# Kernel optimization log

Measured on AMD Instinct MI355X. Metric: run time of the kernel, lower is better.

The kernel has to match this reference:

```python
import jax, jax.numpy as jnp
import numpy as np

N, E, IN, ED, H, C = 50000, 800000, 128, 32, 4, 32
HC = H * C
SCALE = 1.0 / float(np.sqrt(C))


def _seg_softmax(t, idx, n):
    # t: [E, H], idx: [E] target-node ids -> per-segment softmax over incoming edges
    m = jax.ops.segment_max(t, idx, num_segments=n)
    m = jnp.where(jnp.isfinite(m), m, 0.0)
    e = jnp.exp(t - m[idx])
    z = jax.ops.segment_sum(e, idx, num_segments=n)
    return e / (z[idx] + 1e-16)


def setup_inputs() -> dict:
    key = jax.random.key(0)
    ks = jax.random.split(key, 26)
    w = lambda k, shape: (jax.random.normal(k, shape, jnp.float32) * 0.05)
    return {
        "x": jax.random.normal(ks[0], (N, IN), jnp.float32),
        "edge_index": jax.random.randint(ks[1], (2, E), 0, N),
        "edge_attr": jax.random.normal(ks[2], (E, ED), jnp.float32),
        # DifferentialGraphAttention params (dual QK groups + lambda)
        "Wq1": w(ks[3], (HC, IN)), "Wq2": w(ks[4], (HC, IN)),
        "Wk1": w(ks[5], (HC, IN)), "Wk2": w(ks[6], (HC, IN)),
        "Wvd": w(ks[7], (HC, IN)),
        "Wkr1": w(ks[8], (HC, ED)), "Wkr2": w(ks[9], (HC, ED)),
        "Wvrd": w(ks[10], (HC, ED)),
        "Woutd": w(ks[11], (HC, HC)),
        "lam": jnp.float32(0.8),
        # RelationActivationAttention params
        "Wqa": w(ks[12], (HC, IN)), "Wka": w(ks[13], (HC, IN)), "Wva": w(ks[14], (HC, IN)),
        "Wkra": w(ks[15], (HC, ED)), "Wvra": w(ks[16], (HC, ED)),
        "Wouta": w(ks[17], (HC, HC)),
        # Hybrid fusion params
        "Wproj": w(ks[18], (HC, 2 * HC)), "bproj": jnp.zeros((HC,), jnp.float32),
        "Win": w(ks[19], (HC, IN)), "b_in": jnp.zeros((HC,), jnp.float32),
        "rms_w": jnp.ones((HC,), jnp.float32),
    }


def reference(x, edge_index, edge_attr, Wq1, Wq2, Wk1, Wk2, Wvd, Wkr1, Wkr2, Wvrd,
              Woutd, lam, Wqa, Wka, Wva, Wkra, Wvra, Wouta, Wproj, bproj, Win, b_in,
              rms_w):
    src, dst = edge_index[0], edge_index[1]

    def nproj(W):  # [N, HC] -> [N, H, C]
        return (x @ W.T).reshape(N, H, C)

    def eproj(W):  # [E, HC] -> [E, H, C]
        return (edge_attr @ W.T).reshape(E, H, C)

    # ---- differential relation aggregation branch ----
    Q1, Q2, K1, K2, Vd = nproj(Wq1), nproj(Wq2), nproj(Wk1), nproj(Wk2), nproj(Wvd)
    t1 = jnp.sum(Q1[dst] * (K1[src] + eproj(Wkr1)), axis=-1) * SCALE  # [E, H]
    t2 = jnp.sum(Q2[dst] * (K2[src] + eproj(Wkr2)), axis=-1) * SCALE
    a_diff = _seg_softmax(t1, dst, N) - lam * _seg_softmax(t2, dst, N)
    msg_d = (Vd[src] + eproj(Wvrd)) * a_diff[..., None]               # [E, H, C]
    h_aggr = jax.ops.segment_sum(msg_d, dst, num_segments=N).reshape(N, HC) @ Woutd.T

    # ---- relation activation branch ----
    Qa, Ka, Va = nproj(Wqa), nproj(Wka), nproj(Wva)
    ta = jnp.sum(Qa[dst] * (Ka[src] + eproj(Wkra)), axis=-1) * SCALE  # [E, H]
    a_act = _seg_softmax(ta, dst, N)
    msg_a = (Va[src] + eproj(Wvra)) * a_act[..., None]
    h_actv = jax.ops.segment_sum(msg_a, dst, num_segments=N).reshape(N, HC) @ Wouta.T

    # ---- hybrid fusion + residual + RMSNorm ----
    h = jnp.concatenate([h_aggr, h_actv], axis=-1) @ Wproj.T + bproj
    h = h + (x @ Win.T + b_in)
    h = h * jax.lax.rsqrt(jnp.mean(h * h, axis=-1, keepdims=True) + 1e-6) * rms_w
    return h
```

## Files before the change

kernel.cpp:

```cpp
#include <hip/hip_runtime.h>

typedef unsigned short u16;
typedef unsigned int   u32;
typedef _Float16 half8 __attribute__((ext_vector_type(8)));
typedef _Float16 half2v __attribute__((ext_vector_type(2)));
typedef float    f32x4 __attribute__((ext_vector_type(4)));
typedef unsigned int u32x4 __attribute__((ext_vector_type(4)));
typedef int      i32x2 __attribute__((ext_vector_type(2)));

#define NN 50000
#define EE 800000
#define SCALE 0.17677669529663687f
#define NB 49

#define O_WNODET   0ul
#define O_WFT      393216ul
#define O_WF1      524288ul
#define O_WF3      589824ul
#define O_HIST     655360ul
#define O_BSUM     855360ul
#define O_BOFF     855616ul
#define O_OFF      856064ul
#define O_CUR      1056768ul
#define O_PERM     1257472ul
#define O_NODEQ    7657472ul
#define O_NODEKV   97257472ul
#define O_G        161257472ul

__device__ __forceinline__ float fin(float x){
  return (x == x && fabsf(x) < 3e38f) ? x : 0.f;
}
__device__ __forceinline__ u32 packh(float a, float b){
  union{ u32 u; _Float16 h[2]; } cv; cv.h[0]=(_Float16)a; cv.h[1]=(_Float16)b; return cv.u;
}
union H2U { u32 u; half2v h; };
__device__ __forceinline__ half2v h2(u32 u){ H2U c; c.u=u; return c.h; }

__device__ __forceinline__ u32x4 ntl4(const u32* p){
  return __builtin_nontemporal_load((const u32x4*)p);
}
__device__ __forceinline__ f32x4 ntlf4(const float* p){
  return __builtin_nontemporal_load((const f32x4*)p);
}
__device__ __forceinline__ i32x2 ntl2(const i32x2* p){
  return __builtin_nontemporal_load(p);
}

__global__ __launch_bounds__(256) void xcast(const float* __restrict__ x,
                                             _Float16* __restrict__ xh)
{
  int i = blockIdx.x*256 + threadIdx.x;
  size_t b = (size_t)i * 8;
  float4 v0 = *(const float4*)(x + b);
  float4 v1 = *(const float4*)(x + b + 4);
  half8 h;
  h[0]=(_Float16)v0.x; h[1]=(_Float16)v0.y; h[2]=(_Float16)v0.z; h[3]=(_Float16)v0.w;
  h[4]=(_Float16)v1.x; h[5]=(_Float16)v1.y; h[6]=(_Float16)v1.z; h[7]=(_Float16)v1.w;
  *(half8*)(xh + b) = h;
}

__global__ __launch_bounds__(256) void prep1(
    const float* __restrict__ Wq1, const float* __restrict__ Wq2, const float* __restrict__ Wqa,
    const float* __restrict__ Wk1, const float* __restrict__ Wk2, const float* __restrict__ Wka,
    const float* __restrict__ Wvd, const float* __restrict__ Wva, const float* __restrict__ Win,
    const float* __restrict__ Wkr1, const float* __restrict__ Wkr2, const float* __restrict__ Wkra,
    const float* __restrict__ Wproj, const float* __restrict__ Woutd, const float* __restrict__ Wouta,
    _Float16* __restrict__ WnodeT, float* __restrict__ Wf1, float* __restrict__ Wf3)
{
  int job = blockIdx.x*256 + threadIdx.x;
  if (job < 1536*128) {
    int n = job >> 7, kk = job & 127;
    int slot = n >> 7, o = n & 127;
    float val;
    if (slot==3 || slot==4 || slot==5) {
      const float* Wkr = (slot==3)?Wkr1:(slot==4)?Wkr2:Wkra;
      const float* Wq  = (slot==3)?Wq1 :(slot==4)?Wq2 :Wqa;
      int h=o>>5, j=o&31;
      float s=0.f;
      for (int c=0;c<32;c++)
        s += Wkr[(h*32+c)*32 + j] * Wq[(h*32+c)*128 + kk];
      val = s;
    } else {
      const float* W = (slot==0)?Wq1:(slot==1)?Wq2:(slot==2)?Wqa:
                       (slot==6)?Wk1:(slot==7)?Wk2:(slot==8)?Wka:
                       (slot==9)?Wvd:(slot==10)?Wva:Win;
      val = W[o*128 + kk];
    }
    WnodeT[n*128 + kk] = (_Float16)fin(val);
  } else {
    int idx = job - 1536*128;
    int which = idx >> 14;
    int r = idx & 16383;
    int o = r >> 7, v = r & 127;
    const float* Wout = which ? Wouta : Woutd;
    float s=0.f;
    for (int u=0;u<128;u++)
      s += Wproj[o*256 + which*128 + u] * Wout[u*128 + v];
    (which?Wf3:Wf1)[o*128+v] = fin(s);
  }
}

__global__ __launch_bounds__(256) void prep2(
    const float* __restrict__ Wf1, const float* __restrict__ Wf3,
    const float* __restrict__ Wvrd, const float* __restrict__ Wvra,
    _Float16* __restrict__ WfT)
{
  int job = blockIdx.x*256 + threadIdx.x;
  int o = job >> 9, kk = job & 511;
  int seg = kk >> 7, v = kk & 127;
  float val;
  if (seg==0) val = Wf1[o*128+v];
  else if (seg==2) val = Wf3[o*128+v];
  else {
    const float* Wf = (seg==1)?Wf1:Wf3;
    const float* Wv = (seg==1)?Wvrd:Wvra;
    int h=v>>5, j=v&31; float s=0.f;
    for (int c=0;c<32;c++)
      s += Wf[o*128 + h*32 + c] * Wv[(h*32+c)*32 + j];
    val = s;
  }
  WfT[o*512 + kk] = (_Float16)fin(val);
}

__global__ __launch_bounds__(256) void gemm_node(
    const _Float16* __restrict__ xh, const _Float16* __restrict__ WnodeT,
    const float* __restrict__ b_in,
    _Float16* __restrict__ nodeQ, _Float16* __restrict__ nodeKV)
{
  __shared__ _Float16 S[18432];
  _Float16 (*As)[72] = (_Float16(*)[72])S;
  _Float16 (*Bs)[72] = (_Float16(*)[72])(S + 9216);
  int m0 = blockIdx.x * 128;
  int slot = blockIdx.y;
  int n0 = slot * 128;
  int tid = threadIdx.x;
  int lane = tid & 63, wave = tid >> 6;
  int lm = lane & 15, lq = lane >> 4;
  int mbase = wave*32;
  f32x4 acc[2][8];
  #pragma unroll
  for (int i=0;i<2;i++)
    #pragma unroll
    for (int j=0;j<8;j++) acc[i][j] = (f32x4){0.f,0.f,0.f,0.f};

  for (int kt=0; kt<2; kt++){
    int kk0 = kt*64;
    #pragma unroll
    for (int i=0;i<4;i++){
      int c = tid + i*256;
      int row = c >> 3, kc = (c & 7) * 8;
      int grow = m0 + row;
      half8 hv;
      if (grow < NN){
        hv = *(const half8*)(xh + (size_t)grow*128 + kk0 + kc);
      } else {
        #pragma unroll
        for (int j=0;j<8;j++) hv[j] = (_Float16)0.f;
      }
      *(half8*)&As[row][kc] = hv;
      *(half8*)&Bs[row][kc] = *(const half8*)(WnodeT + (size_t)(n0+row)*128 + kk0 + kc);
    }
    __syncthreads();
    #pragma unroll
    for (int ks=0; ks<64; ks+=32){
      half8 a0 = *(half8*)&As[mbase + lm][ks + lq*8];
      half8 a1 = *(half8*)&As[mbase + 16 + lm][ks + lq*8];
      #pragma unroll
      for (int ct=0; ct<8; ct++){
        half8 b = *(half8*)&Bs[ct*16 + lm][ks + lq*8];
        acc[0][ct] = __builtin_amdgcn_mfma_f32_16x16x32_f16(a0, b, acc[0][ct], 0,0,0);
        acc[1][ct] = __builtin_amdgcn_mfma_f32_16x16x32_f16(a1, b, acc[1][ct], 0,0,0);
      }
    }
    __syncthreads();
  }

  #pragma unroll
  for (int rt=0; rt<2; rt++){
    #pragma unroll
    for (int reg=0; reg<4; reg++){
      int row = mbase + rt*16 + lq*4 + reg;
      #pragma unroll
      for (int ct=0; ct<8; ct++){
        int col = ct*16 + lm;
        float bias = (slot == 11) ? b_in[col] : 0.f;
        S[row*136 + col] = (_Float16)fin(acc[rt][ct][reg] + bias);
      }
    }
  }
  __syncthreads();
  #pragma unroll
  for (int i=0;i<8;i++){
    int idx = tid + i*256;
    int row = idx >> 4, c8 = (idx & 15)*8;
    int grow = m0 + row;
    if (grow < NN){
      half8 v = *(half8*)&S[row*136 + c8];
      _Float16* dst = (slot < 6)  ? nodeQ  + (size_t)grow*896 + slot*128 + c8
                    : (slot < 11) ? nodeKV + (size_t)grow*640 + (slot-6)*128 + c8
                                  : nodeQ  + (size_t)grow*896 + 768 + c8;
      *(half8*)dst = v;
    }
  }
}

__global__ __launch_bounds__(256) void hist_k(const int* __restrict__ ei, int* __restrict__ hist){
  int e = blockIdx.x*256 + threadIdx.x;
  int d = ei[EE + e];
  if ((unsigned)d < (unsigned)NN) atomicAdd(&hist[d], 1);
}

__global__ __launch_bounds__(1024) void scan1(const int* __restrict__ hist,
                                              int* __restrict__ loc, int* __restrict__ bsum){
  __shared__ int buf[1024];
  int i = blockIdx.x*1024 + threadIdx.x;
  int v = (i < NN) ? hist[i] : 0;
  buf[threadIdx.x] = v;
  __syncthreads();
  int xv = v;
  for (int s = 1; s < 1024; s <<= 1){
    int t = 0;
    if ((int)threadIdx.x >= s) t = buf[threadIdx.x - s];
    __syncthreads();
    xv += t;
    buf[threadIdx.x] = xv;
    __syncthreads();
  }
  if (i < NN) loc[i] = xv - v;
  if (threadIdx.x == 1023) bsum[blockIdx.x] = xv;
}

__global__ __launch_bounds__(64) void scan2(const int* __restrict__ bsum, int* __restrict__ boff){
  int t = threadIdx.x;
  int v = (t < NB) ? bsum[t] : 0;
  int x = v;
  for (int s = 1; s < 64; s <<= 1){
    int u = __shfl_up(x, s);
    if (t >= s) x += u;
  }
  if (t < NB) boff[t] = x - v;
}

__global__ __launch_bounds__(256) void scatter_k(const int* __restrict__ ei,
                                                 const int* __restrict__ loc, const int* __restrict__ boff,
                                                 int* __restrict__ cur, int2* __restrict__ pe2){
  int e = blockIdx.x*256 + threadIdx.x;
  int d = ei[EE + e];
  if ((unsigned)d >= (unsigned)NN) return;
  int pos = loc[d] + boff[d>>10] + atomicAdd(&cur[d], 1);
  if ((unsigned)pos < (unsigned)EE) pe2[pos] = make_int2(e, ei[e]);
}

__global__ __launch_bounds__(64, 4) void attn_k(
    const i32x2* __restrict__ pe2, const int* __restrict__ hist,
    const int* __restrict__ loc, const int* __restrict__ boff,
    const u32* __restrict__ nfQ, const u32* __restrict__ nfKV,
    const float* __restrict__ ea,
    const float* __restrict__ lamp, u32* __restrict__ G)
{
  int lane = threadIdx.x & 63;
  int node = blockIdx.x;
  if (node >= NN) return;
  int E = lane >> 4;
  int l = lane & 15;
  int h = l >> 2;
  const u32* pd = nfQ + (u32)node * 448u;

  int k = hist[node];
  if (k < 0) k = 0;
  if (k > 64) k = 64;
  int o = loc[node] + boff[node>>10];
  if (o < 0) o = 0;

  int pe_e = 0, pe_s = 0;
  if (k > 0){
    int idxl = (lane < k) ? lane : (k-1);
    i32x2 pl = ntl2(&pe2[o + idxl]);
    pe_e = pl[0]; pe_s = pl[1];
  }

  H2U q1[4], q2[4], qa[4], r1[4], r2[4], ra[4];
  {
    u32x4 a = ntl4(pd +        l*4);
    u32x4 b = ntl4(pd +  64 + l*4);
    u32x4 c = ntl4(pd + 128 + l*4);
    q1[0].u=a[0]; q1[1].u=a[1]; q1[2].u=a[2]; q1[3].u=a[3];
    q2[0].u=b[0]; q2[1].u=b[1]; q2[2].u=b[2]; q2[3].u=b[3];
    qa[0].u=c[0]; qa[1].u=c[1]; qa[2].u=c[2]; qa[3].u=c[3];
    int rb = h*16 + (l&3)*4;
    u32x4 d = ntl4(pd + 192 + rb);
    u32x4 e = ntl4(pd + 256 + rb);
    u32x4 f = ntl4(pd + 320 + rb);
    r1[0].u=d[0]; r1[1].u=d[1]; r1[2].u=d[2]; r1[3].u=d[3];
    r2[0].u=e[0]; r2[1].u=e[1]; r2[2].u=e[2]; r2[3].u=e[3];
    ra[0].u=f[0]; ra[1].u=f[1]; ra[2].u=f[2]; ra[3].u=f[3];
  }

  H2U s1v[4], s2v[4], sav[4], s1e[4], s2e[4], sae[4];
  #pragma unroll
  for (int t=0;t<4;t++){ s1v[t].u=0; s2v[t].u=0; sav[t].u=0; s1e[t].u=0; s2e[t].u=0; sae[t].u=0; }
  float z1=0.f, z2=0.f, za=0.f;

  int iters = (k + 3) >> 2;
  for (int it=0; it<iters; it++){
    int eidx = it*4 + E;
    bool valid = eidx < k;
    int sn = __shfl(pe_s, eidx);
    int ee = __shfl(pe_e, eidx);
    if (!valid){ sn = 0; ee = 0; }
    if ((unsigned)sn >= (unsigned)NN) sn = 0;
    if ((unsigned)ee >= (unsigned)EE) ee = 0;
    const u32* ps = nfKV + (u32)sn * 320u + (u32)(l*4);
    u32x4 K1 = *(const u32x4*)(ps);
    u32x4 K2 = *(const u32x4*)(ps + 64);
    u32x4 KA = *(const u32x4*)(ps + 128);
    u32x4 VD = *(const u32x4*)(ps + 192);
    u32x4 VA = *(const u32x4*)(ps + 256);
    f32x4 ef0 = ntlf4(ea + (size_t)ee*32 + (l&3)*8);
    f32x4 ef1 = ntlf4(ea + (size_t)ee*32 + (l&3)*8 + 4);
    half2v e0 = {(_Float16)ef0[0], (_Float16)ef0[1]};
    half2v e1 = {(_Float16)ef0[2], (_Float16)ef0[3]};
    half2v e2 = {(_Float16)ef1[0], (_Float16)ef1[1]};
    half2v e3 = {(_Float16)ef1[2], (_Float16)ef1[3]};

    half2v p1h = q1[0].h*h2(K1[0]) + q1[1].h*h2(K1[1]) + q1[2].h*h2(K1[2]) + q1[3].h*h2(K1[3])
               + r1[0].h*e0 + r1[1].h*e1 + r1[2].h*e2 + r1[3].h*e3;
    half2v p2h = q2[0].h*h2(K2[0]) + q2[1].h*h2(K2[1]) + q2[2].h*h2(K2[2]) + q2[3].h*h2(K2[3])
               + r2[0].h*e0 + r2[1].h*e1 + r2[2].h*e2 + r2[3].h*e3;
    half2v pah = qa[0].h*h2(KA[0]) + qa[1].h*h2(KA[1]) + qa[2].h*h2(KA[2]) + qa[3].h*h2(KA[3])
               + ra[0].h*e0 + ra[1].h*e1 + ra[2].h*e2 + ra[3].h*e3;

    H2U c1, c2, c3, t;
    c1.h = p1h; c2.h = p2h; c3.h = pah;
    t.u = __shfl_xor(c1.u, 1); c1.h += t.h;
    t.u = __shfl_xor(c2.u, 1); c2.h += t.h;
    t.u = __shfl_xor(c3.u, 1); c3.h += t.h;
    t.u = __shfl_xor(c1.u, 2); c1.h += t.h;
    t.u = __shfl_xor(c2.u, 2); c2.h += t.h;
    t.u = __shfl_xor(c3.u, 2); c3.h += t.h;
    float p1 = (float)c1.h[0] + (float)c1.h[1];
    float p2 = (float)c2.h[0] + (float)c2.h[1];
    float pa = (float)c3.h[0] + (float)c3.h[1];

    float w1 = valid ? __expf(p1*SCALE) : 0.f;
    float w2 = valid ? __expf(p2*SCALE) : 0.f;
    float wa = valid ? __expf(pa*SCALE) : 0.f;
    _Float16 w1f = (_Float16)w1, w2f = (_Float16)w2, waf = (_Float16)wa;
    half2v w1h = {w1f, w1f}, w2h = {w2f, w2f}, wah = {waf, waf};

    s1v[0].h += w1h*h2(VD[0]); s1v[1].h += w1h*h2(VD[1]); s1v[2].h += w1h*h2(VD[2]); s1v[3].h += w1h*h2(VD[3]);
    s2v[0].h += w2h*h2(VD[0]); s2v[1].h += w2h*h2(VD[1]); s2v[2].h += w2h*h2(VD[2]); s2v[3].h += w2h*h2(VD[3]);
    sav[0].h += wah*h2(VA[0]); sav[1].h += wah*h2(VA[1]); sav[2].h += wah*h2(VA[2]); sav[3].h += wah*h2(VA[3]);
    s1e[0].h += w1h*e0; s1e[1].h += w1h*e1; s1e[2].h += w1h*e2; s1e[3].h += w1h*e3;
    s2e[0].h += w2h*e0; s2e[1].h += w2h*e1; s2e[2].h += w2h*e2; s2e[3].h += w2h*e3;
    sae[0].h += wah*e0; sae[1].h += wah*e1; sae[2].h += wah*e2; sae[3].h += wah*e3;
    z1 += w1; z2 += w2; za += wa;
  }

  #pragma unroll
  for (int s=16; s<=32; s<<=1){
    H2U t;
    #pragma unroll
    for (int j=0;j<4;j++){
      t.u = __shfl_xor(s1v[j].u, s); s1v[j].h += t.h;
      t.u = __shfl_xor(s2v[j].u, s); s2v[j].h += t.h;
      t.u = __shfl_xor(sav[j].u, s); sav[j].h += t.h;
      t.u = __shfl_xor(s1e[j].u, s); s1e[j].h += t.h;
      t.u = __shfl_xor(s2e[j].u, s); s2e[j].h += t.h;
      t.u = __shfl_xor(sae[j].u, s); sae[j].h += t.h;
    }
    z1 += __shfl_xor(z1, s); z2 += __shfl_xor(z2, s); za += __shfl_xor(za, s);
  }

  if (E == 0){
    float lamv = lamp[0];
    float i1 = 1.f/(z1+1e-16f), i2 = 1.f/(z2+1e-16f), ia = 1.f/(za+1e-16f);
    u32 gb = (u32)node*256u;
    int rb = h*16 + (l&3)*4;
    #pragma unroll
    for (int t=0;t<4;t++){
      float d0 = fin((float)s1v[t].h[0]*i1 - lamv*((float)s2v[t].h[0]*i2));
      float d1 = fin((float)s1v[t].h[1]*i1 - lamv*((float)s2v[t].h[1]*i2));
      G[gb + l*4 + t] = packh(d0, d1);
      float e0v = fin((float)s1e[t].h[0]*i1 - lamv*((float)s2e[t].h[0]*i2));
      float e1v = fin((float)s1e[t].h[1]*i1 - lamv*((float)s2e[t].h[1]*i2));
      G[gb + 64 + rb + t] = packh(e0v, e1v);
      G[gb + 128 + l*4 + t] = packh(fin((float)sav[t].h[0]*ia), fin((float)sav[t].h[1]*ia));
      G[gb + 192 + rb + t] = packh(fin((float)sae[t].h[0]*ia), fin((float)sae[t].h[1]*ia));
    }
  }
}

__global__ __launch_bounds__(256) void gemm_final(
    const _Float16* __restrict__ Gf, const _Float16* __restrict__ WfT,
    const _Float16* __restrict__ nodeQ,
    const float* __restrict__ bproj, const float* __restrict__ rmsw,
    float* __restrict__ out)
{
  __shared__ _Float16 As[64][72];
  __shared__ _Float16 Bs[128][72];
  __shared__ float bS[128], rS[128];
  int m0 = blockIdx.x * 64;
  int tid = threadIdx.x;
  int lane = tid & 63, wave = tid >> 6;
  int lm = lane & 15, lq = lane >> 4;
  int mbase = wave*16;
  if (tid < 128){ bS[tid] = bproj[tid]; rS[tid] = rmsw[tid]; }
  f32x4 acc[8];
  #pragma unroll
  for (int j=0;j<8;j++) acc[j] = (f32x4){0.f,0.f,0.f,0.f};

  for (int kt=0; kt<8; kt++){
    int kk0 = kt*64;
    #pragma unroll
    for (int i=0;i<2;i++){
      int c = tid + i*256;
      int row = c >> 3, kc = (c & 7) * 8;
      int grow = m0 + row;
      half8 av;
      if (grow < NN){
        av = *(const half8*)(Gf + (size_t)grow*512 + kk0 + kc);
      } else {
        #pragma unroll
        for (int j=0;j<8;j++) av[j] = (_Float16)0.f;
      }
      *(half8*)&As[row][kc] = av;
    }
    #pragma unroll
    for (int i=0;i<4;i++){
      int c = tid + i*256;
      int row = c >> 3, kc = (c & 7) * 8;
      *(half8*)&Bs[row][kc] = *(const half8*)(WfT + (size_t)row*512 + kk0 + kc);
    }
    __syncthreads();
    #pragma unroll
    for (int ks=0; ks<64; ks+=32){
      half8 a0 = *(half8*)&As[mbase + lm][ks + lq*8];
      #pragma unroll
      for (int ct=0; ct<8; ct++){
        half8 b = *(half8*)&Bs[ct*16 + lm][ks + lq*8];
        acc[ct] = __builtin_amdgcn_mfma_f32_16x16x32_f16(a0, b, acc[ct], 0,0,0);
      }
    }
    __syncthreads();
  }
  #pragma unroll
  for (int reg=0; reg<4; reg++){
    int row = m0 + mbase + lq*4 + reg;
    bool ok = row < NN;
    float vals[8]; float ss = 0.f;
    #pragma unroll
    for (int ct=0; ct<8; ct++){
      int col = ct*16 + lm;
      float R = ok ? (float)nodeQ[(size_t)row*896 + 768 + col] : 0.f;
      float v = fin(acc[ct][reg] + bS[col] + R);
      vals[ct] = v; ss += v*v;
    }
    #pragma unroll
    for (int sh=1; sh<16; sh<<=1) ss += __shfl_xor(ss, sh);
    float rstd = rsqrtf(ss*(1.0f/128.f) + 1e-6f);
    if (ok){
      #pragma unroll
      for (int ct=0; ct<8; ct++){
        int col = ct*16 + lm;
        out[(size_t)row*128 + col] = fin(vals[ct]*rstd*rS[col]);
      }
    }
  }
}

extern "C" void kernel_launch(void* const* d_in, const int* in_sizes, int n_in,
                              void* d_out, int out_size, void* d_ws, size_t ws_size,
                              hipStream_t stream)
{
  char* w = (char*)d_ws;
  _Float16* WnodeT = (_Float16*)(w + O_WNODET);
  _Float16* WfT    = (_Float16*)(w + O_WFT);
  float*    Wf1    = (float*)(w + O_WF1);
  float*    Wf3    = (float*)(w + O_WF3);
  int*      hist   = (int*)(w + O_HIST);
  int*      bsum   = (int*)(w + O_BSUM);
  int*      boff   = (int*)(w + O_BOFF);
  int*      loc    = (int*)(w + O_OFF);
  int*      cur    = (int*)(w + O_CUR);
  int2*     pe2    = (int2*)(w + O_PERM);
  _Float16* nodeQ  = (_Float16*)(w + O_NODEQ);
  _Float16* nodeKV = (_Float16*)(w + O_NODEKV);
  _Float16* Gf     = (_Float16*)(w + O_G);
  _Float16* xh     = (_Float16*)(w + O_G);

  const float* x     = (const float*)d_in[0];
  const int*   ei    = (const int*)d_in[1];
  const float* ea    = (const float*)d_in[2];
  const float* Wq1   = (const float*)d_in[3];
  const float* Wq2   = (const float*)d_in[4];
  const float* Wk1   = (const float*)d_in[5];
  const float* Wk2   = (const float*)d_in[6];
  const float* Wvd   = (const float*)d_in[7];
  const float* Wkr1  = (const float*)d_in[8];
  const float* Wkr2  = (const float*)d_in[9];
  const float* Wvrd  = (const float*)d_in[10];
  const float* Woutd = (const float*)d_in[11];
  const float* lam   = (const float*)d_in[12];
  const float* Wqa   = (const float*)d_in[13];
  const float* Wka   = (const float*)d_in[14];
  const float* Wva   = (const float*)d_in[15];
  const float* Wkra  = (const float*)d_in[16];
  const float* Wvra  = (const float*)d_in[17];
  const float* Wouta = (const float*)d_in[18];
  const float* Wproj = (const float*)d_in[19];
  const float* bproj = (const float*)d_in[20];
  const float* Win   = (const float*)d_in[21];
  const float* b_in  = (const float*)d_in[22];
  const float* rmsw  = (const float*)d_in[23];

  (void)hipMemsetAsync(hist, 0, 50000*sizeof(int), stream);
  (void)hipMemsetAsync(cur,  0, 50000*sizeof(int), stream);

  xcast<<<3125, 256, 0, stream>>>(x, xh);
  prep1<<<896, 256, 0, stream>>>(Wq1,Wq2,Wqa, Wk1,Wk2,Wka, Wvd,Wva,Win,
                                 Wkr1,Wkr2,Wkra, Wproj,Woutd,Wouta,
                                 WnodeT, Wf1, Wf3);
  prep2<<<256, 256, 0, stream>>>(Wf1, Wf3, Wvrd, Wvra, WfT);
  gemm_node<<<dim3(391,12), 256, 0, stream>>>(xh, WnodeT, b_in, nodeQ, nodeKV);
  hist_k<<<3125, 256, 0, stream>>>(ei, hist);
  scan1<<<NB, 1024, 0, stream>>>(hist, loc, bsum);
  scan2<<<1, 64, 0, stream>>>(bsum, boff);
  scatter_k<<<3125, 256, 0, stream>>>(ei, loc, boff, cur, pe2);
  attn_k<<<50000, 64, 0, stream>>>((const i32x2*)pe2, hist, loc, boff, (const u32*)nodeQ,
                                   (const u32*)nodeKV, ea, lam, (u32*)Gf);
  gemm_final<<<782, 256, 0, stream>>>(Gf, WfT, nodeQ, bproj, rmsw, (float*)d_out);
}
```

Baseline: 563.5 us.

## Fold counter zeroing into xcast, split attention launch, stage final output via LDS

The two hipMemsetAsync calls are removed, and zeroing of hist and cur now happens inside the xcast kernel. The attention kernel is launched as four quarter-grid launches with a node base offset. The final GEMM writes normalized rows into shared memory, which reuses the A/B tile buffer, and then stores them to global memory as coalesced 16-byte vectors. These changes aim to cut memset launch overhead and uncoalesced scalar output stores, at the cost of an extra barrier and three extra kernel launches.

```diff
diff --git a/kernel.cpp b/kernel.cpp
--- a/kernel.cpp
+++ b/kernel.cpp
@@ -47,9 +47,11 @@
 }
 
 __global__ __launch_bounds__(256) void xcast(const float* __restrict__ x,
-                                             _Float16* __restrict__ xh)
+                                             _Float16* __restrict__ xh,
+                                             int* __restrict__ hist, int* __restrict__ cur)
 {
   int i = blockIdx.x*256 + threadIdx.x;
+  if (i < NN){ hist[i] = 0; cur[i] = 0; }
   size_t b = (size_t)i * 8;
   float4 v0 = *(const float4*)(x + b);
   float4 v1 = *(const float4*)(x + b + 4);
@@ -256,10 +258,10 @@
     const int* __restrict__ loc, const int* __restrict__ boff,
     const u32* __restrict__ nfQ, const u32* __restrict__ nfKV,
     const float* __restrict__ ea,
-    const float* __restrict__ lamp, u32* __restrict__ G)
+    const float* __restrict__ lamp, u32* __restrict__ G, int nbase)
 {
   int lane = threadIdx.x & 63;
-  int node = blockIdx.x;
+  int node = nbase + blockIdx.x;
   if (node >= NN) return;
   int E = lane >> 4;
   int l = lane & 15;
@@ -397,8 +399,10 @@
     const float* __restrict__ bproj, const float* __restrict__ rmsw,
     float* __restrict__ out)
 {
-  __shared__ _Float16 As[64][72];
-  __shared__ _Float16 Bs[128][72];
+  __shared__ char SS[34816];
+  _Float16 (*As)[72] = (_Float16(*)[72])SS;
+  _Float16 (*Bs)[72] = (_Float16(*)[72])(SS + 9216);
+  float* Sf = (float*)SS;
   __shared__ float bS[128], rS[128];
   int m0 = blockIdx.x * 64;
   int tid = threadIdx.x;
@@ -446,7 +450,8 @@
   }
   #pragma unroll
   for (int reg=0; reg<4; reg++){
-    int row = m0 + mbase + lq*4 + reg;
+    int rowl = mbase + lq*4 + reg;
+    int row = m0 + rowl;
     bool ok = row < NN;
     float vals[8]; float ss = 0.f;
     #pragma unroll
@@ -459,12 +464,21 @@
     #pragma unroll
     for (int sh=1; sh<16; sh<<=1) ss += __shfl_xor(ss, sh);
     float rstd = rsqrtf(ss*(1.0f/128.f) + 1e-6f);
-    if (ok){
-      #pragma unroll
-      for (int ct=0; ct<8; ct++){
-        int col = ct*16 + lm;
-        out[(size_t)row*128 + col] = fin(vals[ct]*rstd*rS[col]);
-      }
+    #pragma unroll
+    for (int ct=0; ct<8; ct++){
+      int col = ct*16 + lm;
+      Sf[rowl*132 + col] = fin(vals[ct]*rstd*rS[col]);
+    }
+  }
+  __syncthreads();
+  #pragma unroll
+  for (int i=0;i<8;i++){
+    int idx = tid + i*256;
+    int rowl = idx >> 5, c4 = (idx & 31) * 4;
+    int grow = m0 + rowl;
+    if (grow < NN){
+      f32x4 v = *(f32x4*)&Sf[rowl*132 + c4];
+      *(f32x4*)(out + (size_t)grow*128 + c4) = v;
     }
   }
 }
@@ -514,10 +528,7 @@
   const float* b_in  = (const float*)d_in[22];
   const float* rmsw  = (const float*)d_in[23];
 
-  (void)hipMemsetAsync(hist, 0, 50000*sizeof(int), stream);
-  (void)hipMemsetAsync(cur,  0, 50000*sizeof(int), stream);
-
-  xcast<<<3125, 256, 0, stream>>>(x, xh);
+  xcast<<<3125, 256, 0, stream>>>(x, xh, hist, cur);
   prep1<<<896, 256, 0, stream>>>(Wq1,Wq2,Wqa, Wk1,Wk2,Wka, Wvd,Wva,Win,
                                  Wkr1,Wkr2,Wkra, Wproj,Woutd,Wouta,
                                  WnodeT, Wf1, Wf3);
@@ -527,7 +538,13 @@
   scan1<<<NB, 1024, 0, stream>>>(hist, loc, bsum);
   scan2<<<1, 64, 0, stream>>>(bsum, boff);
   scatter_k<<<3125, 256, 0, stream>>>(ei, loc, boff, cur, pe2);
-  attn_k<<<50000, 64, 0, stream>>>((const i32x2*)pe2, hist, loc, boff, (const u32*)nodeQ,
-                                   (const u32*)nodeKV, ea, lam, (u32*)Gf);
+  attn_k<<<12500, 64, 0, stream>>>((const i32x2*)pe2, hist, loc, boff, (const u32*)nodeQ,
+                                   (const u32*)nodeKV, ea, lam, (u32*)Gf, 0);
+  attn_k<<<12500, 64, 0, stream>>>((const i32x2*)pe2, hist, loc, boff, (const u32*)nodeQ,
+                                   (const u32*)nodeKV, ea, lam, (u32*)Gf, 12500);
+  attn_k<<<12500, 64, 0, stream>>>((const i32x2*)pe2, hist, loc, boff, (const u32*)nodeQ,
+                                   (const u32*)nodeKV, ea, lam, (u32*)Gf, 25000);
+  attn_k<<<12500, 64, 0, stream>>>((const i32x2*)pe2, hist, loc, boff, (const u32*)nodeQ,
+                                   (const u32*)nodeKV, ea, lam, (u32*)Gf, 37500);
   gemm_final<<<782, 256, 0, stream>>>(Gf, WfT, nodeQ, bproj, rmsw, (float*)d_out);
 }
```

Measured after the change: 581.5 us. 1.03x slower.
